# Kernel tuning notes

Measured on AMD Instinct MI355X. Metric: run time of the kernel, lower is better.

The kernel has to match this reference:

```python
import jax, jax.numpy as jnp
import numpy as np

# Problem sizes
N, D, B = 4096, 2048, 64  # nodes, feature dim, sequential samples
# LARFDSSOM hyperparameters (from __init__ defaults)
A_T = 0.3          # activation threshold
DSBETA = 1e-4      # moving-average rate
E_B = 0.5          # winner learning rate
E_N = 0.01 * E_B   # neighbor learning rate (e_n is multiplied by e_b in __init__)
EPS_DS = 0.01      # relevance smoothing


def setup_inputs() -> dict:
    key = jax.random.key(0)
    k0, k1, k2, k3, k4 = jax.random.split(key, 5)
    return {
        "x": jax.random.uniform(k0, (B, D), jnp.float32),
        "weights": jax.random.uniform(k1, (N, D), jnp.float32),
        "moving_avg": jax.random.uniform(k2, (N, D), jnp.float32),
        "relevances": jax.random.uniform(k3, (N, D), jnp.float32),
        "wins": jnp.zeros((N,), jnp.float32),
        "neighbors": jax.random.randint(k4, (N, N), 0, 2) > 0,
    }


def _som_steps(x, weights, moving_avg, relevances, wins, neighbors):
    """Sequential LARFDSSOM update_map over B samples (codebook at max size,
    so the add_node branch is structurally impossible and the per-sample step
    is either 'update winner + neighbors' or a no-op)."""
    node_ids = jnp.arange(weights.shape[0])

    def step(state, w):
        W, M, R, wn = state
        diff = w[None, :] - W                          # [N, D]
        # weighted_distance + activation
        dists = jnp.sum(R * diff * diff, axis=1)       # [N]
        rel_sum = jnp.sum(R, axis=1)                   # [N]
        act = rel_sum / (rel_sum + dists + 1e-7)
        winner = jnp.argmax(act)
        do_upd = act[winner] >= A_T                    # else no-op (codebook full)
        is_winner = node_ids == winner
        is_nb = neighbors[winner] & (~is_winner)
        # per-node learning rate: e_b for winner, e_n for neighbors, 0 otherwise
        lr = jnp.where(is_winner, E_B, jnp.where(is_nb, E_N, 0.0))[:, None]  # [N, 1]
        # update_node (vectorized over all nodes, masked below)
        dist_abs = jnp.abs(diff)
        M_new = lr * DSBETA * dist_abs + (1.0 - lr * DSBETA) * M
        mx = jnp.max(M_new, axis=1, keepdims=True)
        mn = jnp.min(M_new, axis=1, keepdims=True)
        av = jnp.mean(M_new, axis=1, keepdims=True)
        denom = EPS_DS * (mx - mn)
        # denom == 0 -> original produces NaN then sets relevance to 1.0
        arg = jnp.clip((M_new - av) / jnp.where(denom == 0.0, 1.0, denom), -80.0, 80.0)
        R_new = jnp.where(denom == 0.0, 1.0, 1.0 / (1.0 + jnp.exp(arg)))
        W_new = W + lr * diff
        m = (do_upd & (lr[:, 0] > 0.0))[:, None]       # rows actually touched
        W = jnp.where(m, W_new, W)
        M = jnp.where(m, M_new, M)
        R = jnp.where(m, R_new, R)
        wn = wn + jnp.where(is_winner & do_upd, 1.0, 0.0)
        return (W, M, R, wn), None

    (W, M, R, wn), _ = jax.lax.scan(step, (weights, moving_avg, relevances, wins), x)
    return W


def reference(x, weights, moving_avg, relevances, wins, neighbors):
    return _som_steps(x, weights, moving_avg, relevances, wins, neighbors)
```

## Files before the change

### kernel.cpp

```cpp
#include <hip/hip_runtime.h>
#include <cstddef>

#define NN 4096
#define DD 2048
#define BB 64
#define RPB 8
#define NBLK (NN / RPB)

constexpr float kAT     = 0.3f;
constexpr float kDSBETA = 1e-4f;
constexpr float kEB     = 0.5f;
constexpr float kEN     = 0.005f;
constexpr float kEPS    = 0.01f;

__device__ __forceinline__ float wave_sum_f(float v) {
#pragma unroll
    for (int o = 32; o; o >>= 1) v += __shfl_xor(v, o, 64);
    return v;
}
__device__ __forceinline__ double wave_sum_d(double v) {
#pragma unroll
    for (int o = 32; o; o >>= 1) v += __shfl_xor(v, o, 64);
    return v;
}
__device__ __forceinline__ float wave_max_f(float v) {
#pragma unroll
    for (int o = 32; o; o >>= 1) v = fmaxf(v, __shfl_xor(v, o, 64));
    return v;
}
__device__ __forceinline__ float wave_min_f(float v) {
#pragma unroll
    for (int o = 32; o; o >>= 1) v = fminf(v, __shfl_xor(v, o, 64));
    return v;
}
__device__ __forceinline__ unsigned long long wave_max_u64(unsigned long long v) {
#pragma unroll
    for (int o = 32; o; o >>= 1) {
        const unsigned long long u = __shfl_xor(v, o, 64);
        v = (u > v) ? u : v;
    }
    return v;
}

__global__ void detect_nb(const unsigned char* __restrict__ nb, unsigned* __restrict__ flag) {
    unsigned v = 0;
    const int i0 = threadIdx.x * 256;
    for (int i = 0; i < 256; i++) {
        const int idx = i0 + i;
        if ((idx & 3) != 0) v |= nb[idx];
    }
    if (v != 0) atomicOr(flag, 1u);
}

__global__ __launch_bounds__(256, 2) void som_persist(
    const float* __restrict__ x,
    const float* __restrict__ W0,
    const float* __restrict__ M0,
    const float* __restrict__ R0,
    const unsigned char* __restrict__ nbb,
    const unsigned* __restrict__ flag,
    float* __restrict__ Wout,
    unsigned long long* __restrict__ keys,
    unsigned long long* __restrict__ wkey)
{
    const int tid  = threadIdx.x;
    const int wid  = tid >> 6;
    const int lane = tid & 63;
    const int bid  = (int)blockIdx.x;
    const int n0   = bid * RPB;
    const int col  = tid * 8;

    __shared__ double sdd[2][RPB][4];
    __shared__ float  sf[3][4];
    __shared__ unsigned long long skk[RPB];
    __shared__ unsigned long long sKey;

    const bool nb_byte = (*flag != 0);

    float w[RPB][8], r[RPB][8], m[RPB][8], xcur[8], xnext[8];

#pragma unroll
    for (int row = 0; row < RPB; ++row) {
        const size_t base = (size_t)(n0 + row) * DD + col;
        *(float4*)(&w[row][0]) = *(const float4*)(W0 + base);
        *(float4*)(&w[row][4]) = *(const float4*)(W0 + base + 4);
        *(float4*)(&r[row][0]) = *(const float4*)(R0 + base);
        *(float4*)(&r[row][4]) = *(const float4*)(R0 + base + 4);
        *(float4*)(&m[row][0]) = *(const float4*)(M0 + base);
        *(float4*)(&m[row][4]) = *(const float4*)(M0 + base + 4);
    }
    *(float4*)(xcur)     = *(const float4*)(x + col);
    *(float4*)(xcur + 4) = *(const float4*)(x + col + 4);

    auto post_key = [&](int slot) {
#pragma unroll
        for (int row = 0; row < RPB; ++row) {
            double pd = 0.0, ps = 0.0;
#pragma unroll
            for (int j = 0; j < 8; ++j) {
                const double d  = (double)xcur[j] - (double)w[row][j];
                const double rj = (double)r[row][j];
                pd += rj * d * d;
                ps += rj;
            }
            pd = wave_sum_d(pd); ps = wave_sum_d(ps);
            if (lane == 0) { sdd[0][row][wid] = pd; sdd[1][row][wid] = ps; }
        }
        __syncthreads();
        if (tid < RPB) {
            const int row = tid;
            const double td = sdd[0][row][0] + sdd[0][row][1] + sdd[0][row][2] + sdd[0][row][3];
            const double tr = sdd[1][row][0] + sdd[1][row][1] + sdd[1][row][2] + sdd[1][row][3];
            const double act = tr / (tr + td + 1e-7);
            const unsigned long long ab = (unsigned long long)__double_as_longlong(act);
            skk[row] = (ab & ~0xFFFULL) | (unsigned long long)(4095 - (n0 + row));
        }
        __syncthreads();
        if (tid == 0) {
            unsigned long long k = skk[0];
#pragma unroll
            for (int i = 1; i < RPB; ++i) k = (skk[i] > k) ? skk[i] : k;
            __hip_atomic_store(&keys[(size_t)slot * NBLK + bid], k,
                               __ATOMIC_RELEASE, __HIP_MEMORY_SCOPE_AGENT);
        }
        __syncthreads();
    };

    post_key(0);
    *(float4*)(xnext)     = *(const float4*)(x + DD + col);
    *(float4*)(xnext + 4) = *(const float4*)(x + DD + 4 + col);

    for (int t = 0; t < BB; ++t) {
        if (bid == 0 && wid == 0) {
            const unsigned long long* kt = keys + (size_t)t * NBLK;
            int it = 0;
            while (true) {
                bool ok = true;
                unsigned long long mx = 0;
#pragma unroll
                for (int i = 0; i < NBLK / 64; ++i) {
                    const unsigned long long v = __hip_atomic_load(
                        &kt[lane + 64 * i], __ATOMIC_RELAXED, __HIP_MEMORY_SCOPE_AGENT);
                    ok &= (v != 0ULL);
                    mx = (v > mx) ? v : mx;
                }
                if (__all(ok) || ++it > 4000000) {
                    mx = wave_max_u64(mx);
                    if (lane < 8)
                        __hip_atomic_store(&wkey[((size_t)t * 8 + lane) * 8], mx,
                                           __ATOMIC_RELEASE, __HIP_MEMORY_SCOPE_AGENT);
                    break;
                }
                __builtin_amdgcn_s_sleep(1);
            }
        }
        if (tid == 0) {
            unsigned long long k = 0;
            int it = 0;
            while (true) {
                k = __hip_atomic_load(&wkey[((size_t)t * 8 + (bid & 7)) * 8],
                                      __ATOMIC_RELAXED, __HIP_MEMORY_SCOPE_AGENT);
                if (k != 0ULL || ++it > 4000000) break;
                __builtin_amdgcn_s_sleep(4);
            }
            sKey = k;
        }
        __syncthreads();
        const unsigned long long k = sKey;
        __syncthreads();
        const double act_w = __longlong_as_double((long long)(k & ~0xFFFULL));
        const int winner   = 4095 - (int)(k & 0xFFFULL);

        if (act_w >= (double)kAT) {
            bool isnb[RPB];
            if (nb_byte) {
                const unsigned long long nbw =
                    *(const unsigned long long*)(nbb + (size_t)winner * NN + n0);
#pragma unroll
                for (int i = 0; i < RPB; ++i) isnb[i] = ((nbw >> (8 * i)) & 0xFFULL) != 0;
            } else {
                const uint4* p = (const uint4*)((const int*)nbb + (size_t)winner * NN + n0);
                const uint4 a = p[0], b = p[1];
                isnb[0] = a.x != 0; isnb[1] = a.y != 0; isnb[2] = a.z != 0; isnb[3] = a.w != 0;
                isnb[4] = b.x != 0; isnb[5] = b.y != 0; isnb[6] = b.z != 0; isnb[7] = b.w != 0;
            }
#pragma unroll
            for (int row = 0; row < RPB; ++row) {
                const int n = n0 + row;
                const float lr = (n == winner) ? kEB : (isnb[row] ? kEN : 0.0f);
                if (lr != 0.0f) {
                    const float c1 = lr * kDSBETA;
                    const float c2 = 1.0f - c1;
                    float psum = 0.0f, pmx = -INFINITY, pmn = INFINITY;
#pragma unroll
                    for (int j = 0; j < 8; ++j) {
                        const float d  = xcur[j] - w[row][j];
                        const float mv = c1 * fabsf(d) + c2 * m[row][j];
                        w[row][j] += lr * d;
                        m[row][j] = mv;
                        psum += mv;
                        pmx = fmaxf(pmx, mv);
                        pmn = fminf(pmn, mv);
                    }
                    psum = wave_sum_f(psum); pmx = wave_max_f(pmx); pmn = wave_min_f(pmn);
                    if (lane == 0) { sf[0][wid] = psum; sf[1][wid] = pmx; sf[2][wid] = pmn; }
                    __syncthreads();
                    const float ts  = sf[0][0] + sf[0][1] + sf[0][2] + sf[0][3];
                    const float tmx = fmaxf(fmaxf(sf[1][0], sf[1][1]), fmaxf(sf[1][2], sf[1][3]));
                    const float tmn = fminf(fminf(sf[2][0], sf[2][1]), fminf(sf[2][2], sf[2][3]));
                    __syncthreads();
                    const float av    = ts * (1.0f / (float)DD);
                    const float denom = kEPS * (tmx - tmn);
                    if (denom == 0.0f) {
#pragma unroll
                        for (int j = 0; j < 8; ++j) r[row][j] = 1.0f;
                    } else {
#pragma unroll
                        for (int j = 0; j < 8; ++j) {
                            float a = (m[row][j] - av) / denom;
                            a = fminf(fmaxf(a, -80.0f), 80.0f);
                            r[row][j] = 1.0f / (1.0f + expf(a));
                        }
                    }
                }
            }
        }

        if (t < BB - 1) {
#pragma unroll
            for (int j = 0; j < 8; ++j) xcur[j] = xnext[j];
            post_key(t + 1);
            if (t < BB - 2) {
                const size_t xb = (size_t)(t + 2) * DD + col;
                *(float4*)(xnext)     = *(const float4*)(x + xb);
                *(float4*)(xnext + 4) = *(const float4*)(x + xb + 4);
            }
        }
    }

#pragma unroll
    for (int row = 0; row < RPB; ++row) {
        const size_t base = (size_t)(n0 + row) * DD + col;
        *(float4*)(Wout + base)     = *(float4*)(&w[row][0]);
        *(float4*)(Wout + base + 4) = *(float4*)(&w[row][4]);
    }
}

__global__ __launch_bounds__(256) void som_step(
    const float* __restrict__ x_upd, const float* __restrict__ x_act,
    float* __restrict__ W, float* __restrict__ M, float* __restrict__ R,
    const void* __restrict__ nb, const unsigned* __restrict__ flag,
    const unsigned long long* __restrict__ part_upd,
    unsigned long long* __restrict__ part_act)
{
    const int n   = blockIdx.x;
    const int tid = threadIdx.x;
    __shared__ float  sred[3][4];
    __shared__ double sredd[2][4];

    float lr = 0.0f;
    if (part_upd != nullptr) {
        unsigned long long k = part_upd[(size_t)(tid & 63) * 8];
        k = wave_max_u64(k);
        const double act_w = __longlong_as_double((long long)(k & ~0xFFFULL));
        const int winner   = 4095 - (int)(k & 0xFFFULL);
        if (act_w >= (double)kAT) {
            if (n == winner) lr = kEB;
            else {
                const size_t off = (size_t)winner * NN + n;
                const bool isnb = (*flag != 0)
                    ? (((const unsigned char*)nb)[off] != 0)
                    : (((const int*)nb)[off] != 0);
                if (isnb) lr = kEN;
            }
        }
    }
    const bool next = (x_act != nullptr);
    if (lr == 0.0f && !next) return;

    const size_t rowoff = (size_t)n * DD + (size_t)tid * 8;
    const size_t xoff   = (size_t)tid * 8;
    float w[8], r[8];
    *(float4*)(w)     = *(const float4*)(W + rowoff);
    *(float4*)(w + 4) = *(const float4*)(W + rowoff + 4);

    if (lr != 0.0f) {
        float m[8], xu[8], mnew[8];
        *(float4*)(m)      = *(const float4*)(M + rowoff);
        *(float4*)(m + 4)  = *(const float4*)(M + rowoff + 4);
        *(float4*)(xu)     = *(const float4*)(x_upd + xoff);
        *(float4*)(xu + 4) = *(const float4*)(x_upd + xoff + 4);
        const float c1 = lr * kDSBETA, c2 = 1.0f - c1;
        float psum = 0.0f, pmx = -INFINITY, pmn = INFINITY;
#pragma unroll
        for (int j = 0; j < 8; j++) {
            const float d = xu[j] - w[j];
            w[j] += lr * d;
            const float mv = c1 * fabsf(d) + c2 * m[j];
            mnew[j] = mv; psum += mv;
            pmx = fmaxf(pmx, mv); pmn = fminf(pmn, mv);
        }
        psum = wave_sum_f(psum); pmx = wave_max_f(pmx); pmn = wave_min_f(pmn);
        const int wid = tid >> 6, lane = tid & 63;
        if (lane == 0) { sred[0][wid] = psum; sred[1][wid] = pmx; sred[2][wid] = pmn; }
        __syncthreads();
        const float ts  = sred[0][0] + sred[0][1] + sred[0][2] + sred[0][3];
        const float tmx = fmaxf(fmaxf(sred[1][0], sred[1][1]), fmaxf(sred[1][2], sred[1][3]));
        const float tmn = fminf(fminf(sred[2][0], sred[2][1]), fminf(sred[2][2], sred[2][3]));
        __syncthreads();
        const float av = ts * (1.0f / (float)DD);
        const float denom = kEPS * (tmx - tmn);
        if (denom == 0.0f) {
#pragma unroll
            for (int j = 0; j < 8; j++) r[j] = 1.0f;
        } else {
#pragma unroll
            for (int j = 0; j < 8; j++) {
                float a = (mnew[j] - av) / denom;
                a = fminf(fmaxf(a, -80.0f), 80.0f);
                r[j] = 1.0f / (1.0f + expf(a));
            }
        }
        *(float4*)(W + rowoff)     = *(float4*)(w);
        *(float4*)(W + rowoff + 4) = *(float4*)(w + 4);
        *(float4*)(M + rowoff)     = *(float4*)(mnew);
        *(float4*)(M + rowoff + 4) = *(float4*)(mnew + 4);
        *(float4*)(R + rowoff)     = *(float4*)(r);
        *(float4*)(R + rowoff + 4) = *(float4*)(r + 4);
    } else {
        *(float4*)(r)     = *(const float4*)(R + rowoff);
        *(float4*)(r + 4) = *(const float4*)(R + rowoff + 4);
    }

    if (next) {
        float xn[8];
        *(float4*)(xn)     = *(const float4*)(x_act + xoff);
        *(float4*)(xn + 4) = *(const float4*)(x_act + xoff + 4);
        double pd = 0.0, ps = 0.0;
#pragma unroll
        for (int j = 0; j < 8; j++) {
            const double d  = (double)xn[j] - (double)w[j];
            const double rj = (double)r[j];
            pd += rj * d * d; ps += rj;
        }
        pd = wave_sum_d(pd); ps = wave_sum_d(ps);
        const int wid = tid >> 6, lane = tid & 63;
        if (lane == 0) { sredd[0][wid] = pd; sredd[1][wid] = ps; }
        __syncthreads();
        if (tid == 0) {
            const double td = sredd[0][0] + sredd[0][1] + sredd[0][2] + sredd[0][3];
            const double tr = sredd[1][0] + sredd[1][1] + sredd[1][2] + sredd[1][3];
            const double act = tr / (tr + td + 1e-7);
            const unsigned long long ab = (unsigned long long)__double_as_longlong(act);
            const unsigned long long kk = (ab & ~0xFFFULL) | (unsigned long long)(4095 - n);
            atomicMax(&part_act[(size_t)(n & 63) * 8], kk);
        }
    }
}

extern "C" void kernel_launch(void* const* d_in, const int* in_sizes, int n_in,
                              void* d_out, int out_size, void* d_ws, size_t ws_size,
                              hipStream_t stream) {
    const float*         x   = (const float*)d_in[0];
    const float*         W0  = (const float*)d_in[1];
    float*               M   = (float*)d_in[2];
    float*               R   = (float*)d_in[3];
    const unsigned char* nbb = (const unsigned char*)d_in[5];
    float*               W   = (float*)d_out;

    const size_t regA = (size_t)66 * 64 * 8 * sizeof(unsigned long long);
    const size_t regB = (size_t)BB * 8 * 8 * sizeof(unsigned long long);
    unsigned long long* keys  = (unsigned long long*)d_ws;
    unsigned long long* wkey  = (unsigned long long*)((char*)d_ws + regA);
    unsigned*           flagp = (unsigned*)((char*)d_ws + regA + regB);

    hipMemsetAsync(d_ws, 0, regA + regB + 64, stream);
    detect_nb<<<1, 256, 0, stream>>>(nbb, flagp);

    int occ = 0;
    hipError_t qerr = hipOccupancyMaxActiveBlocksPerMultiprocessor(
        &occ, (const void*)som_persist, 256, 0);
    if (qerr == hipSuccess && occ >= 2) {
        som_persist<<<NBLK, 256, 0, stream>>>(x, W0, M, R, nbb, flagp, W, keys, wkey);
        return;
    }

    unsigned long long* part = keys;
    hipMemcpyAsync(W, W0, sizeof(float) * (size_t)NN * DD, hipMemcpyDeviceToDevice, stream);
    som_step<<<NN, 256, 0, stream>>>(nullptr, x, W, M, R, nbb, flagp, nullptr, part);
    for (int t = 0; t < BB; t++) {
        const float* xu = x + (size_t)t * DD;
        const float* xa = (t < BB - 1) ? (x + (size_t)(t + 1) * DD) : nullptr;
        const unsigned long long* pu = part + (size_t)t * 64 * 8;
        unsigned long long*       pa = (t < BB - 1) ? (part + (size_t)(t + 1) * 64 * 8) : nullptr;
        som_step<<<NN, 256, 0, stream>>>(xu, xa, W, M, R, nbb, flagp, pu, pa);
    }
}
```

Baseline: 1.669 ms.

## Have every block poll all keys directly and batch per-row reductions under one barrier

Each block's first wave now scans all per-block keys itself to find the winner, replacing the two-level scheme where block 0 reduced the keys and broadcast a winner key for the others to poll. The per-row update reductions now write to a per-row shared array and share a single barrier instead of two barriers per updated row. Key stores become relaxed and a few trailing barriers are dropped. This shortens the global handoff chain and cuts intra-block barriers, at the cost of more global polling traffic across 512 blocks and weaker memory ordering that could let a block read a stale key.

```diff
diff --git a/kernel.cpp b/kernel.cpp
--- a/kernel.cpp
+++ b/kernel.cpp
@@ -60,8 +60,7 @@
     const unsigned char* __restrict__ nbb,
     const unsigned* __restrict__ flag,
     float* __restrict__ Wout,
-    unsigned long long* __restrict__ keys,
-    unsigned long long* __restrict__ wkey)
+    unsigned long long* __restrict__ keys)
 {
     const int tid  = threadIdx.x;
     const int wid  = tid >> 6;
@@ -71,7 +70,7 @@
     const int col  = tid * 8;
 
     __shared__ double sdd[2][RPB][4];
-    __shared__ float  sf[3][4];
+    __shared__ float  sup[3][RPB][4];
     __shared__ unsigned long long skk[RPB];
     __shared__ unsigned long long sKey;
 
@@ -121,9 +120,8 @@
 #pragma unroll
             for (int i = 1; i < RPB; ++i) k = (skk[i] > k) ? skk[i] : k;
             __hip_atomic_store(&keys[(size_t)slot * NBLK + bid], k,
-                               __ATOMIC_RELEASE, __HIP_MEMORY_SCOPE_AGENT);
-        }
-        __syncthreads();
+                               __ATOMIC_RELAXED, __HIP_MEMORY_SCOPE_AGENT);
+        }
     };
 
     post_key(0);
@@ -131,12 +129,13 @@
     *(float4*)(xnext + 4) = *(const float4*)(x + DD + 4 + col);
 
     for (int t = 0; t < BB; ++t) {
-        if (bid == 0 && wid == 0) {
+        if (wid == 0) {
             const unsigned long long* kt = keys + (size_t)t * NBLK;
+            unsigned long long mx = 0;
             int it = 0;
             while (true) {
                 bool ok = true;
-                unsigned long long mx = 0;
+                mx = 0;
 #pragma unroll
                 for (int i = 0; i < NBLK / 64; ++i) {
                     const unsigned long long v = __hip_atomic_load(
@@ -144,50 +143,39 @@
                     ok &= (v != 0ULL);
                     mx = (v > mx) ? v : mx;
                 }
-                if (__all(ok) || ++it > 4000000) {
-                    mx = wave_max_u64(mx);
-                    if (lane < 8)
-                        __hip_atomic_store(&wkey[((size_t)t * 8 + lane) * 8], mx,
-                                           __ATOMIC_RELEASE, __HIP_MEMORY_SCOPE_AGENT);
-                    break;
-                }
+                if (__all(ok) || ++it > 4000000) break;
                 __builtin_amdgcn_s_sleep(1);
             }
-        }
-        if (tid == 0) {
-            unsigned long long k = 0;
-            int it = 0;
-            while (true) {
-                k = __hip_atomic_load(&wkey[((size_t)t * 8 + (bid & 7)) * 8],
-                                      __ATOMIC_RELAXED, __HIP_MEMORY_SCOPE_AGENT);
-                if (k != 0ULL || ++it > 4000000) break;
-                __builtin_amdgcn_s_sleep(4);
-            }
-            sKey = k;
+            mx = wave_max_u64(mx);
+            if (lane == 0) sKey = mx;
         }
         __syncthreads();
         const unsigned long long k = sKey;
-        __syncthreads();
         const double act_w = __longlong_as_double((long long)(k & ~0xFFFULL));
         const int winner   = 4095 - (int)(k & 0xFFFULL);
 
         if (act_w >= (double)kAT) {
-            bool isnb[RPB];
+            float lrs[RPB];
             if (nb_byte) {
                 const unsigned long long nbw =
                     *(const unsigned long long*)(nbb + (size_t)winner * NN + n0);
 #pragma unroll
-                for (int i = 0; i < RPB; ++i) isnb[i] = ((nbw >> (8 * i)) & 0xFFULL) != 0;
+                for (int i = 0; i < RPB; ++i)
+                    lrs[i] = (n0 + i == winner) ? kEB
+                           : ((((nbw >> (8 * i)) & 0xFFULL) != 0) ? kEN : 0.0f);
             } else {
                 const uint4* p = (const uint4*)((const int*)nbb + (size_t)winner * NN + n0);
                 const uint4 a = p[0], b = p[1];
-                isnb[0] = a.x != 0; isnb[1] = a.y != 0; isnb[2] = a.z != 0; isnb[3] = a.w != 0;
-                isnb[4] = b.x != 0; isnb[5] = b.y != 0; isnb[6] = b.z != 0; isnb[7] = b.w != 0;
-            }
+                const bool nz[RPB] = { a.x != 0, a.y != 0, a.z != 0, a.w != 0,
+                                       b.x != 0, b.y != 0, b.z != 0, b.w != 0 };
+#pragma unroll
+                for (int i = 0; i < RPB; ++i)
+                    lrs[i] = (n0 + i == winner) ? kEB : (nz[i] ? kEN : 0.0f);
+            }
+
 #pragma unroll
             for (int row = 0; row < RPB; ++row) {
-                const int n = n0 + row;
-                const float lr = (n == winner) ? kEB : (isnb[row] ? kEN : 0.0f);
+                const float lr = lrs[row];
                 if (lr != 0.0f) {
                     const float c1 = lr * kDSBETA;
                     const float c2 = 1.0f - c1;
@@ -203,12 +191,24 @@
                         pmn = fminf(pmn, mv);
                     }
                     psum = wave_sum_f(psum); pmx = wave_max_f(pmx); pmn = wave_min_f(pmn);
-                    if (lane == 0) { sf[0][wid] = psum; sf[1][wid] = pmx; sf[2][wid] = pmn; }
-                    __syncthreads();
-                    const float ts  = sf[0][0] + sf[0][1] + sf[0][2] + sf[0][3];
-                    const float tmx = fmaxf(fmaxf(sf[1][0], sf[1][1]), fmaxf(sf[1][2], sf[1][3]));
-                    const float tmn = fminf(fminf(sf[2][0], sf[2][1]), fminf(sf[2][2], sf[2][3]));
-                    __syncthreads();
+                    if (lane == 0) {
+                        sup[0][row][wid] = psum;
+                        sup[1][row][wid] = pmx;
+                        sup[2][row][wid] = pmn;
+                    }
+                }
+            }
+            __syncthreads();
+
+#pragma unroll
+            for (int row = 0; row < RPB; ++row) {
+                if (lrs[row] != 0.0f) {
+                    const float ts  = sup[0][row][0] + sup[0][row][1]
+                                    + sup[0][row][2] + sup[0][row][3];
+                    const float tmx = fmaxf(fmaxf(sup[1][row][0], sup[1][row][1]),
+                                            fmaxf(sup[1][row][2], sup[1][row][3]));
+                    const float tmn = fminf(fminf(sup[2][row][0], sup[2][row][1]),
+                                            fminf(sup[2][row][2], sup[2][row][3]));
                     const float av    = ts * (1.0f / (float)DD);
                     const float denom = kEPS * (tmx - tmn);
                     if (denom == 0.0f) {
@@ -369,19 +369,17 @@
     float*               W   = (float*)d_out;
 
     const size_t regA = (size_t)66 * 64 * 8 * sizeof(unsigned long long);
-    const size_t regB = (size_t)BB * 8 * 8 * sizeof(unsigned long long);
     unsigned long long* keys  = (unsigned long long*)d_ws;
-    unsigned long long* wkey  = (unsigned long long*)((char*)d_ws + regA);
-    unsigned*           flagp = (unsigned*)((char*)d_ws + regA + regB);
-
-    hipMemsetAsync(d_ws, 0, regA + regB + 64, stream);
+    unsigned*           flagp = (unsigned*)((char*)d_ws + regA);
+
+    hipMemsetAsync(d_ws, 0, regA + 64, stream);
     detect_nb<<<1, 256, 0, stream>>>(nbb, flagp);
 
     int occ = 0;
     hipError_t qerr = hipOccupancyMaxActiveBlocksPerMultiprocessor(
         &occ, (const void*)som_persist, 256, 0);
     if (qerr == hipSuccess && occ >= 2) {
-        som_persist<<<NBLK, 256, 0, stream>>>(x, W0, M, R, nbb, flagp, W, keys, wkey);
+        som_persist<<<NBLK, 256, 0, stream>>>(x, W0, M, R, nbb, flagp, W, keys);
         return;
     }
 
```

After: 1.687 ms. About the same (+1.1%).
